# Performance work log

Measured on AMD Instinct MI355X. Metric: run time of the kernel, lower is better.

The kernel has to match this reference:

```python
import jax, jax.numpy as jnp
import numpy as np

EPS = 1e-6


def setup_inputs() -> dict:
    key = jax.random.key(0)
    k1, k2 = jax.random.split(key)
    T, B, D, n = 2048, 16, 1024, 64
    x = jax.random.normal(k1, (T, B, D), dtype=jnp.float32)
    S0 = jnp.zeros((B, n, n), dtype=jnp.float32)
    G0 = jnp.zeros((B, n, n), dtype=jnp.float32)
    # xavier-uniform-ish init for each n x D block of the fused projection
    limit = float(np.sqrt(6.0 / (n + D)))
    W_kvqm = jax.random.uniform(k2, (4 * n, D), dtype=jnp.float32, minval=-limit, maxval=limit)
    b_s_gate = jnp.full((n,), 2.0, dtype=jnp.float32)
    b_g_gate = jnp.full((n,), 2.5, dtype=jnp.float32)
    return {"x": x, "S0": S0, "G0": G0, "W_kvqm": W_kvqm,
            "b_s_gate": b_s_gate, "b_g_gate": b_g_gate}


def _e81_forward(x, S0, G0, W_kvqm, b_s_gate, b_g_gate):
    T, B, D = x.shape
    n = b_s_gate.shape[0]
    # Fused projection: [T, B, 4n]
    proj = jnp.einsum('tbd,nd->tbn', x, W_kvqm)
    k_all, v_all, q_all, m_all = jnp.split(proj, 4, axis=-1)

    bs = b_s_gate[None, :, None]  # broadcast over [B, n(row), n(col)]
    bg = b_g_gate[None, :, None]

    def step(carry, kvqm):
        S, G = carry
        k, v, q, m_vec = kvqm  # each [B, n]
        k_norm = k / (jnp.linalg.norm(k, axis=-1, keepdims=True) + EPS)
        m_norm = m_vec / (jnp.linalg.norm(m_vec, axis=-1, keepdims=True) + EPS)

        gate_S = jax.nn.sigmoid(G + bs)
        s_retrieved = jnp.einsum('bij,bj->bi', S, k_norm)
        s_delta = v - s_retrieved
        S = gate_S * S + jnp.einsum('bi,bj->bij', s_delta, k_norm)

        gate_G = jax.nn.sigmoid(S + bg)
        g_retrieved = jnp.einsum('bij,bj->bi', G, m_norm)
        g_delta = s_delta - g_retrieved
        G = gate_G * G + jnp.einsum('bi,bj->bij', g_delta, m_norm)

        Sq = jnp.einsum('bij,bj->bi', S, q)
        out = Sq * jax.nn.silu(Sq)  # self-gated output
        return (S, G), out

    (S, G), output = jax.lax.scan(step, (S0, G0), (k_all, v_all, q_all, m_all))
    return output, S, G


def reference(x, S0, G0, W_kvqm, b_s_gate, b_g_gate):
    return _e81_forward(x, S0, G0, W_kvqm, b_s_gate, b_g_gate)
```

## Files before the change

### kernel.cpp

```cpp
#include <hip/hip_runtime.h>
#include <hip/hip_bf16.h>

#define EPS 1e-6f

typedef float f32x4 __attribute__((ext_vector_type(4)));
typedef short bf16x8 __attribute__((ext_vector_type(8)));

__device__ __forceinline__ unsigned f2bf(float x) {
  __hip_bfloat16 h = __float2bfloat16(x);
  return *reinterpret_cast<unsigned short*>(&h);
}
__device__ __forceinline__ unsigned split_pack(float x) {
  unsigned hi = f2bf(x);
  unsigned short hs = (unsigned short)hi;
  float hif = __bfloat162float(*reinterpret_cast<__hip_bfloat16*>(&hs));
  unsigned lo = f2bf(x - hif);
  return (lo << 16) | hi;
}

union FragCast { unsigned u[4]; bf16x8 v; };

constexpr int GBM = 128, GBK = 32;

__global__ __launch_bounds__(512) void proj_gemm_mfma(
    const float* __restrict__ A,
    const float* __restrict__ Bw,
    float* __restrict__ C,
    int M, int K) {
  __shared__ unsigned As[GBM * GBK];
  __shared__ unsigned Bs[256 * GBK];

  const int tid  = threadIdx.x;
  const int lane = tid & 63;
  const int wid  = tid >> 6;
  const int m0   = blockIdx.x * GBM;
  const int wm   = (wid >> 2) * 64;
  const int wn   = (wid & 3) * 64;

  const int ar = tid >> 2, ak = (tid & 3) * 8;
  const int br = tid >> 1, bk = (tid & 1) * 16;

  f32x4 acc[4][4] = {};

  for (int k0 = 0; k0 < K; k0 += GBK) {
    {
      const float* src = &A[(size_t)(m0 + ar) * K + k0 + ak];
      float4 v0 = *(const float4*)(src);
      float4 v1 = *(const float4*)(src + 4);
      unsigned p0[4] = {split_pack(v0.x), split_pack(v0.y),
                        split_pack(v0.z), split_pack(v0.w)};
      unsigned p1[4] = {split_pack(v1.x), split_pack(v1.y),
                        split_pack(v1.z), split_pack(v1.w)};
      unsigned swz  = (unsigned)(ar & 7) << 4;
      char* base = (char*)As + ar * 128;
      *(uint4*)(base + (((unsigned)ak * 4) ^ swz))       = *(uint4*)p0;
      *(uint4*)(base + (((unsigned)(ak + 4) * 4) ^ swz)) = *(uint4*)p1;
    }
    {
      const float* src = &Bw[(size_t)br * K + k0 + bk];
      unsigned swz = (unsigned)(br & 7) << 4;
      char* base = (char*)Bs + br * 128;
#pragma unroll
      for (int q = 0; q < 4; ++q) {
        float4 v = *(const float4*)(src + q * 4);
        unsigned p[4] = {split_pack(v.x), split_pack(v.y),
                         split_pack(v.z), split_pack(v.w)};
        *(uint4*)(base + (((unsigned)(bk + q * 4) * 4) ^ swz)) = *(uint4*)p;
      }
    }
    __syncthreads();

    unsigned ah[4][4], al[4][4];
    const unsigned ko = ((unsigned)(lane >> 4)) * 16;
#pragma unroll
    for (int mf = 0; mf < 4; ++mf) {
      int r = wm + mf * 16 + (lane & 15);
      unsigned swz = (unsigned)(r & 7) << 4;
      char* base = (char*)As + r * 128;
      uint4 w0 = *(uint4*)(base + (ko ^ swz));
      uint4 w1 = *(uint4*)(base + ((64 + ko) ^ swz));
      ah[mf][0] = __builtin_amdgcn_perm(w0.y, w0.x, 0x05040100);
      al[mf][0] = __builtin_amdgcn_perm(w0.y, w0.x, 0x07060302);
      ah[mf][1] = __builtin_amdgcn_perm(w0.w, w0.z, 0x05040100);
      al[mf][1] = __builtin_amdgcn_perm(w0.w, w0.z, 0x07060302);
      ah[mf][2] = __builtin_amdgcn_perm(w1.y, w1.x, 0x05040100);
      al[mf][2] = __builtin_amdgcn_perm(w1.y, w1.x, 0x07060302);
      ah[mf][3] = __builtin_amdgcn_perm(w1.w, w1.z, 0x05040100);
      al[mf][3] = __builtin_amdgcn_perm(w1.w, w1.z, 0x07060302);
    }

#pragma unroll
    for (int nf = 0; nf < 4; ++nf) {
      int r = wn + nf * 16 + (lane & 15);
      unsigned swz = (unsigned)(r & 7) << 4;
      char* base = (char*)Bs + r * 128;
      uint4 w0 = *(uint4*)(base + (ko ^ swz));
      uint4 w1 = *(uint4*)(base + ((64 + ko) ^ swz));
      FragCast bh, bl;
      bh.u[0] = __builtin_amdgcn_perm(w0.y, w0.x, 0x05040100);
      bl.u[0] = __builtin_amdgcn_perm(w0.y, w0.x, 0x07060302);
      bh.u[1] = __builtin_amdgcn_perm(w0.w, w0.z, 0x05040100);
      bl.u[1] = __builtin_amdgcn_perm(w0.w, w0.z, 0x07060302);
      bh.u[2] = __builtin_amdgcn_perm(w1.y, w1.x, 0x05040100);
      bl.u[2] = __builtin_amdgcn_perm(w1.y, w1.x, 0x07060302);
      bh.u[3] = __builtin_amdgcn_perm(w1.w, w1.z, 0x05040100);
      bl.u[3] = __builtin_amdgcn_perm(w1.w, w1.z, 0x07060302);
#pragma unroll
      for (int mf = 0; mf < 4; ++mf) {
        FragCast fah, fal;
        fah.u[0] = ah[mf][0]; fah.u[1] = ah[mf][1];
        fah.u[2] = ah[mf][2]; fah.u[3] = ah[mf][3];
        fal.u[0] = al[mf][0]; fal.u[1] = al[mf][1];
        fal.u[2] = al[mf][2]; fal.u[3] = al[mf][3];
        acc[mf][nf] = __builtin_amdgcn_mfma_f32_16x16x32_bf16(
            fah.v, bh.v, acc[mf][nf], 0, 0, 0);
        acc[mf][nf] = __builtin_amdgcn_mfma_f32_16x16x32_bf16(
            fah.v, bl.v, acc[mf][nf], 0, 0, 0);
        acc[mf][nf] = __builtin_amdgcn_mfma_f32_16x16x32_bf16(
            fal.v, bh.v, acc[mf][nf], 0, 0, 0);
      }
    }
    __syncthreads();
  }

#pragma unroll
  for (int mf = 0; mf < 4; ++mf) {
    int row = m0 + wm + mf * 16 + (lane >> 4) * 4;
#pragma unroll
    for (int nf = 0; nf < 4; ++nf) {
      int col = wn + nf * 16 + (lane & 15);
#pragma unroll
      for (int r = 0; r < 4; ++r)
        C[(size_t)(row + r) * 256 + col] = acc[mf][nf][r];
    }
  }
}

template <int CTRL>
__device__ __forceinline__ float dpp_mov(float v) {
  return __int_as_float(
      __builtin_amdgcn_update_dpp(0, __float_as_int(v), CTRL, 0xF, 0xF, true));
}

__device__ __forceinline__ float wave_sum_all(float v) {
  v += dpp_mov<0x121>(v);
  v += dpp_mov<0x122>(v);
  v += dpp_mov<0x124>(v);
  v += dpp_mov<0x128>(v);
  v += dpp_mov<0x142>(v);
  v += dpp_mov<0x143>(v);
  return __int_as_float(__builtin_amdgcn_readlane(__float_as_int(v), 63));
}

__device__ __forceinline__ float reduce16(float v) {
  v += dpp_mov<0x121>(v);
  v += dpp_mov<0x122>(v);
  v += dpp_mov<0x124>(v);
  v += dpp_mov<0x128>(v);
  return v;
}

#define L2E 1.4426950408889634f
__device__ __forceinline__ float sigm_b(float x, float nb) {
  float t = __builtin_amdgcn_exp2f(fmaf(x, -L2E, nb));
  return __builtin_amdgcn_rcpf(1.0f + t);
}
__device__ __forceinline__ float sigm(float x) {
  float t = __builtin_amdgcn_exp2f(x * -L2E);
  return __builtin_amdgcn_rcpf(1.0f + t);
}

__global__ __launch_bounds__(256) void normalize_km(float* __restrict__ proj,
                                                    int rows) {
  const int w = blockIdx.x * 4 + (threadIdx.x >> 6);
  const int lane = threadIdx.x & 63;
  if (w >= rows) return;
  float* p = proj + (size_t)w * 256;
  const int src = 16 * (lane & 3) + (lane >> 2);
  float k = p[src];
  float q = p[128 + src];
  float m = p[192 + src];
  float nk = sqrtf(wave_sum_all(k * k)) + EPS;
  float nm = sqrtf(wave_sum_all(m * m)) + EPS;
  p[lane]       = k * __builtin_amdgcn_rcpf(nk);
  p[128 + lane] = q;
  p[192 + lane] = m * __builtin_amdgcn_rcpf(nm);
}

__global__ __launch_bounds__(64) void e81_scan(
    const float* __restrict__ proj,
    const float* __restrict__ S0,
    const float* __restrict__ G0,
    const float* __restrict__ bsg,
    const float* __restrict__ bgg,
    float* __restrict__ dout,
    int T) {
  const int lane = threadIdx.x;
  const int l = lane & 15;
  const int g = lane >> 4;
  const int b  = blockIdx.x >> 4;
  const int wb = blockIdx.x & 15;
  const int row = wb * 4 + g;

  const size_t sgbase = ((size_t)(b * 64 + row)) * 64 + l;
  float S[4], G[4];
#pragma unroll
  for (int e = 0; e < 4; ++e) {
    S[e] = S0[sgbase + 16 * e];
    G[e] = G0[sgbase + 16 * e];
  }
  const float nbs = -bsg[row] * L2E;
  const float nbg = -bgg[row] * L2E;

  float* outp = dout;
  float* Sout = dout + (size_t)T * 16 * 64;
  float* Gout = Sout + 16 * 64 * 64;

  const float* p = proj + b * 256;
  float4 k = *(const float4*)(p + 4 * l);
  float4 q = *(const float4*)(p + 128 + 4 * l);
  float4 m = *(const float4*)(p + 192 + 4 * l);
  float  v = p[64 + row];

  for (int t = 0; t < T; ++t) {
    const float* pn = (t + 1 < T) ? (p + 16 * 256) : p;
    float4 kn = *(const float4*)(pn + 4 * l);
    float4 qn = *(const float4*)(pn + 128 + 4 * l);
    float4 mn = *(const float4*)(pn + 192 + 4 * l);
    float  vn = pn[64 + row];

    float sr = S[0] * k.x;
    sr = fmaf(S[1], k.y, sr);
    sr = fmaf(S[2], k.z, sr);
    sr = fmaf(S[3], k.w, sr);
    sr = reduce16(sr);
    float gr = G[0] * m.x;
    gr = fmaf(G[1], m.y, gr);
    gr = fmaf(G[2], m.z, gr);
    gr = fmaf(G[3], m.w, gr);
    gr = reduce16(gr);

    float sdelta = v - sr;
    S[0] = fmaf(sigm_b(G[0], nbs), S[0], sdelta * k.x);
    S[1] = fmaf(sigm_b(G[1], nbs), S[1], sdelta * k.y);
    S[2] = fmaf(sigm_b(G[2], nbs), S[2], sdelta * k.z);
    S[3] = fmaf(sigm_b(G[3], nbs), S[3], sdelta * k.w);

    float gd = sdelta - gr;
    G[0] = fmaf(sigm_b(S[0], nbg), G[0], gd * m.x);
    G[1] = fmaf(sigm_b(S[1], nbg), G[1], gd * m.y);
    G[2] = fmaf(sigm_b(S[2], nbg), G[2], gd * m.z);
    G[3] = fmaf(sigm_b(S[3], nbg), G[3], gd * m.w);

    float sq = S[0] * q.x;
    sq = fmaf(S[1], q.y, sq);
    sq = fmaf(S[2], q.z, sq);
    sq = fmaf(S[3], q.w, sq);
    sq = reduce16(sq);

    if (l == 0)
      outp[(((size_t)t << 4) + b) * 64 + row] = sq * sq * sigm(sq);

    k = kn; q = qn; m = mn; v = vn;
    p = pn;
  }

#pragma unroll
  for (int e = 0; e < 4; ++e) {
    Sout[sgbase + 16 * e] = S[e];
    Gout[sgbase + 16 * e] = G[e];
  }
}

extern "C" void kernel_launch(void* const* d_in, const int* in_sizes, int n_in,
                              void* d_out, int out_size, void* d_ws, size_t ws_size,
                              hipStream_t stream) {
  const float* x  = (const float*)d_in[0];
  const float* S0 = (const float*)d_in[1];
  const float* G0 = (const float*)d_in[2];
  const float* W  = (const float*)d_in[3];
  const float* bs = (const float*)d_in[4];
  const float* bg = (const float*)d_in[5];
  float* out = (float*)d_out;
  float* proj = (float*)d_ws;

  const int B = 16, D = 1024;
  const int T = in_sizes[0] / (B * D);
  const int M = T * B;

  proj_gemm_mfma<<<dim3(M / GBM), 512, 0, stream>>>(x, W, proj, M, D);

  normalize_km<<<dim3(M / 4), 256, 0, stream>>>(proj, M);

  e81_scan<<<dim3(256), 64, 0, stream>>>(proj, S0, G0, bs, bg, out, T);
}
```

Baseline: 885.5 us.

## Unroll scan by two, reorder gate math, and move output activation to separate kernel

The recurrent scan loop is unrolled by two time steps with double prefetch of the projected inputs. The S-gate sigmoids are computed before the reductions, and the Sq reduction is moved ahead of the G update, giving more independent work to hide latency on the serial chain. The self-gated output activation is moved out of the scan into a separate elementwise kernel. This shortens the critical path per step at the cost of an extra launch and an extra pass over the output. The loop assumes T is even.

```diff
diff --git a/kernel.cpp b/kernel.cpp
--- a/kernel.cpp
+++ b/kernel.cpp
@@ -187,6 +187,8 @@
   p[192 + lane] = m * __builtin_amdgcn_rcpf(nm);
 }
 
+#define PSTR 4096
+
 __global__ __launch_bounds__(64) void e81_scan(
     const float* __restrict__ proj,
     const float* __restrict__ S0,
@@ -216,59 +218,88 @@
   float* Sout = dout + (size_t)T * 16 * 64;
   float* Gout = Sout + 16 * 64 * 64;
 
-  const float* p = proj + b * 256;
-  float4 k = *(const float4*)(p + 4 * l);
-  float4 q = *(const float4*)(p + 128 + 4 * l);
-  float4 m = *(const float4*)(p + 192 + 4 * l);
-  float  v = p[64 + row];
-
-  for (int t = 0; t < T; ++t) {
-    const float* pn = (t + 1 < T) ? (p + 16 * 256) : p;
-    float4 kn = *(const float4*)(pn + 4 * l);
-    float4 qn = *(const float4*)(pn + 128 + 4 * l);
-    float4 mn = *(const float4*)(pn + 192 + 4 * l);
-    float  vn = pn[64 + row];
-
-    float sr = S[0] * k.x;
-    sr = fmaf(S[1], k.y, sr);
-    sr = fmaf(S[2], k.z, sr);
-    sr = fmaf(S[3], k.w, sr);
-    sr = reduce16(sr);
-    float gr = G[0] * m.x;
-    gr = fmaf(G[1], m.y, gr);
-    gr = fmaf(G[2], m.z, gr);
-    gr = fmaf(G[3], m.w, gr);
-    gr = reduce16(gr);
-
-    float sdelta = v - sr;
-    S[0] = fmaf(sigm_b(G[0], nbs), S[0], sdelta * k.x);
-    S[1] = fmaf(sigm_b(G[1], nbs), S[1], sdelta * k.y);
-    S[2] = fmaf(sigm_b(G[2], nbs), S[2], sdelta * k.z);
-    S[3] = fmaf(sigm_b(G[3], nbs), S[3], sdelta * k.w);
-
-    float gd = sdelta - gr;
-    G[0] = fmaf(sigm_b(S[0], nbg), G[0], gd * m.x);
-    G[1] = fmaf(sigm_b(S[1], nbg), G[1], gd * m.y);
-    G[2] = fmaf(sigm_b(S[2], nbg), G[2], gd * m.z);
-    G[3] = fmaf(sigm_b(S[3], nbg), G[3], gd * m.w);
-
-    float sq = S[0] * q.x;
-    sq = fmaf(S[1], q.y, sq);
-    sq = fmaf(S[2], q.z, sq);
-    sq = fmaf(S[3], q.w, sq);
-    sq = reduce16(sq);
-
-    if (l == 0)
-      outp[(((size_t)t << 4) + b) * 64 + row] = sq * sq * sigm(sq);
-
-    k = kn; q = qn; m = mn; v = vn;
-    p = pn;
-  }
+  const float* pA = proj + b * 256;
+  const float* pB = pA + PSTR;
+  float4 kA = *(const float4*)(pA + 4 * l);
+  float4 qA = *(const float4*)(pA + 128 + 4 * l);
+  float4 mA = *(const float4*)(pA + 192 + 4 * l);
+  float  vA = pA[64 + row];
+  float4 kB = *(const float4*)(pB + 4 * l);
+  float4 qB = *(const float4*)(pB + 128 + 4 * l);
+  float4 mB = *(const float4*)(pB + 192 + 4 * l);
+  float  vB = pB[64 + row];
+
+#define STEP(k_, q_, m_, v_, tidx)                                       \
+  {                                                                      \
+                     \
+    float gs0 = sigm_b(G[0], nbs), gs1 = sigm_b(G[1], nbs);              \
+    float gs2 = sigm_b(G[2], nbs), gs3 = sigm_b(G[3], nbs);              \
+    float sr = S[0] * k_.x;                                              \
+    sr = fmaf(S[1], k_.y, sr);                                           \
+    sr = fmaf(S[2], k_.z, sr);                                           \
+    sr = fmaf(S[3], k_.w, sr);                                           \
+    sr = reduce16(sr);                                                   \
+    float gr = G[0] * m_.x;                                              \
+    gr = fmaf(G[1], m_.y, gr);                                           \
+    gr = fmaf(G[2], m_.z, gr);                                           \
+    gr = fmaf(G[3], m_.w, gr);                                           \
+    gr = reduce16(gr);                                                   \
+    float sdelta = v_ - sr;                                              \
+    S[0] = fmaf(gs0, S[0], sdelta * k_.x);                               \
+    S[1] = fmaf(gs1, S[1], sdelta * k_.y);                               \
+    S[2] = fmaf(gs2, S[2], sdelta * k_.z);                               \
+    S[3] = fmaf(gs3, S[3], sdelta * k_.w);                               \
+     \
+    float sq = S[0] * q_.x;                                              \
+    sq = fmaf(S[1], q_.y, sq);                                           \
+    sq = fmaf(S[2], q_.z, sq);                                           \
+    sq = fmaf(S[3], q_.w, sq);                                           \
+    sq = reduce16(sq);                                                   \
+    float gd = sdelta - gr;                                              \
+    G[0] = fmaf(sigm_b(S[0], nbg), G[0], gd * m_.x);                     \
+    G[1] = fmaf(sigm_b(S[1], nbg), G[1], gd * m_.y);                     \
+    G[2] = fmaf(sigm_b(S[2], nbg), G[2], gd * m_.z);                     \
+    G[3] = fmaf(sigm_b(S[3], nbg), G[3], gd * m_.w);                     \
+    if (l == 0) outp[(((size_t)(tidx) << 4) + b) * 64 + row] = sq;       \
+  }
+
+  for (int t = 0; t < T; t += 2) {
+    const float* pA2 = (t + 2 < T) ? (pA + 2 * PSTR) : pA;
+    const float* pB2 = (t + 3 < T) ? (pB + 2 * PSTR) : pB;
+    float4 kA2 = *(const float4*)(pA2 + 4 * l);
+    float4 qA2 = *(const float4*)(pA2 + 128 + 4 * l);
+    float4 mA2 = *(const float4*)(pA2 + 192 + 4 * l);
+    float  vA2 = pA2[64 + row];
+    float4 kB2 = *(const float4*)(pB2 + 4 * l);
+    float4 qB2 = *(const float4*)(pB2 + 128 + 4 * l);
+    float4 mB2 = *(const float4*)(pB2 + 192 + 4 * l);
+    float  vB2 = pB2[64 + row];
+
+    STEP(kA, qA, mA, vA, t)
+    STEP(kB, qB, mB, vB, t + 1)
+
+    kA = kA2; qA = qA2; mA = mA2; vA = vA2; pA = pA2;
+    kB = kB2; qB = qB2; mB = mB2; vB = vB2; pB = pB2;
+  }
+#undef STEP
 
 #pragma unroll
   for (int e = 0; e < 4; ++e) {
     Sout[sgbase + 16 * e] = S[e];
     Gout[sgbase + 16 * e] = G[e];
+  }
+}
+
+__global__ __launch_bounds__(256) void out_act(float* __restrict__ o, int n4) {
+  int i = blockIdx.x * 256 + threadIdx.x;
+  if (i < n4) {
+    float4 x = *(float4*)(o + 4 * i);
+    float4 r;
+    r.x = x.x * x.x * sigm(x.x);
+    r.y = x.y * x.y * sigm(x.y);
+    r.z = x.z * x.z * sigm(x.z);
+    r.w = x.w * x.w * sigm(x.w);
+    *(float4*)(o + 4 * i) = r;
   }
 }
 
@@ -293,4 +324,7 @@
   normalize_km<<<dim3(M / 4), 256, 0, stream>>>(proj, M);
 
   e81_scan<<<dim3(256), 64, 0, stream>>>(proj, S0, G0, bs, bg, out, T);
-}
+
+  const int n4 = T * B * 64 / 4;
+  out_act<<<dim3((n4 + 255) / 256), 256, 0, stream>>>(out, n4);
+}
```

Result: faster. 757.2 us (-14.5%).
